# Kernel optimization log

Measured on AMD Instinct MI355X. Metric: run time of the kernel, lower is better.

Reference implementation:

```python
import jax, jax.numpy as jnp
import numpy as np
import math

FS = 9          # gaussian filter_size
STD = 1.0
LOW = 0.1       # min(threshold1, threshold2)
HIGH = 0.3      # max(threshold1, threshold2)
PAD_G = FS // 2


def _gauss_window(M, std):
    # scipy.signal.windows.gaussian: exp(-0.5*(n/std)^2), n centered, unnormalized
    n = np.arange(M, dtype=np.float64) - (M - 1) / 2.0
    return np.exp(-0.5 * (n / std) ** 2).astype(np.float32)


def _conv(x, w, pad):
    # torch F.conv2d == cross-correlation, NCHW / OIHW
    return jax.lax.conv_general_dilated(
        x, w, window_strides=(1, 1), padding=pad,
        dimension_numbers=("NCHW", "OIHW", "NCHW"))


def setup_inputs() -> dict:
    key = jax.random.key(0)
    img = jax.random.uniform(key, (8, 3, 512, 512), dtype=jnp.float32)
    g = _gauss_window(FS, STD)
    gauss_h = jnp.asarray(g[None, None, None, :])          # [1,1,1,9]
    gauss_v = jnp.asarray(g[None, None, :, None])          # [1,1,9,1]
    sobel_h = jnp.array([[[[1., 0., -1.], [2., 0., -2.], [1., 0., -1.]]]], dtype=jnp.float32)
    sobel_v = jnp.array([[[[1., 2., 1.], [0., 0., 0.], [-1., -2., -1.]]]], dtype=jnp.float32)
    d = np.zeros((8, 1, 3, 3), dtype=np.float32)
    d[:, 0, 1, 1] = 1.0
    # neighbor positions (row, col) for the -1 tap, per directional channel
    neigh = [(1, 2), (2, 2), (2, 1), (2, 0), (1, 0), (0, 0), (0, 1), (0, 2)]
    for k, (r, c) in enumerate(neigh):
        d[k, 0, r, c] = -1.0
    directional = jnp.asarray(d)                            # [8,1,3,3]
    connect = jnp.array([[[[1., 1., 1.], [1., 0., 1.], [1., 1., 1.]]]], dtype=jnp.float32)
    return {"img": img, "gauss_h": gauss_h, "gauss_v": gauss_v,
            "sobel_h": sobel_h, "sobel_v": sobel_v,
            "directional": directional, "connect": connect}


def reference(img, gauss_h, gauss_v, sobel_h, sobel_v, directional, connect):
    B, C, H, W = img.shape
    x = img.reshape(B * C, 1, H, W)  # per-channel 1-in/1-out convs, batched
    blur = _conv(_conv(x, gauss_h, [(0, 0), (PAD_G, PAD_G)]),
                 gauss_v, [(PAD_G, PAD_G), (0, 0)])
    gx = _conv(blur, sobel_h, [(1, 1), (1, 1)]).reshape(B, C, H, W)
    gy = _conv(blur, sobel_v, [(1, 1), (1, 1)]).reshape(B, C, H, W)

    # sum of per-channel magnitudes, [B,1,H,W]
    grad_mag = jnp.sqrt(gx * gx + gy * gy).sum(axis=1, keepdims=True)
    ori = jnp.arctan2(gy.sum(axis=1, keepdims=True),
                      gx.sum(axis=1, keepdims=True)) * (180.0 / math.pi) + 180.0
    ori = jnp.round(ori / 45.0) * 45.0

    all_filtered = _conv(grad_mag, directional, [(1, 1), (1, 1)])  # [B,8,H,W]

    pixel_count = B * H * W
    pr = jnp.arange(pixel_count, dtype=jnp.int32)
    flat = all_filtered.reshape(-1)
    # faithful replication of the original's flat linear-index gather
    k_pos = ((ori / 45.0) % 8.0).reshape(-1).astype(jnp.int32)
    k_neg = ((ori / 45.0 + 4.0) % 8.0).reshape(-1).astype(jnp.int32)
    pos = flat[k_pos * pixel_count + pr].reshape(B, 1, H, W)
    neg = flat[k_neg * pixel_count + pr].reshape(B, 1, H, W)

    is_max = jnp.minimum(pos, neg) > 0.0
    thin = jnp.where(is_max, grad_mag, 0.0)

    t = jnp.where(thin < LOW, 0.0, thin)
    higher = thin > HIGH
    t = jnp.where(higher, 1.0, t)
    connect_map = _conv(higher.astype(jnp.float32), connect, [(1, 1), (1, 1)])
    middle = (thin >= LOW) & (thin <= HIGH)
    t = jnp.where(middle, 0.0, t)
    connect_map = jnp.where(middle, connect_map, 0.0)
    t = jnp.where(connect_map > 0.0, 1.0, t)
    # zero borders
    t = t.at[..., 0, :].set(0.0)
    t = t.at[..., -1, :].set(0.0)
    t = t.at[..., :, 0].set(0.0)
    t = t.at[..., :, -1].set(0.0)
    return (t > 0.0).astype(jnp.float32)
```

## Files before the change

### kernel.cpp

```cpp
#include <hip/hip_runtime.h>
#include <math.h>

#define HH 512
#define WW 512
#define NB 8
#define NC 3
#define HW (HH*WW)

#define RSTRIP 16
#define CSTRIP 62
#define NROWS (HH/RSTRIP)
#define NCOLS ((WW + CSTRIP - 1)/CSTRIP)

__global__ __launch_bounds__(64) void canny_gm_kernel(
    const float* __restrict__ img, const float* __restrict__ gwin,
    double* __restrict__ GM, unsigned char* __restrict__ KP)
{
    const int lane = threadIdx.x;
    const int cs   = blockIdx.x % NCOLS;
    const int rs   = blockIdx.x / NCOLS;
    const int b    = blockIdx.y;

    const int R0 = rs * RSTRIP;
    const int c0 = cs * CSTRIP - 1;
    const int cl = c0 + lane;

    double g[9];
#pragma unroll
    for (int k = 0; k < 9; ++k) g[k] = (double)gwin[k];

    int cidx[9]; bool cmask[9];
#pragma unroll
    for (int k = 0; k < 9; ++k) {
        int cc = cl - 4 + k;
        cmask[k] = ((unsigned)cc < (unsigned)WW);
        int cc2 = cc < 0 ? 0 : cc;
        cidx[k] = cc2 > (WW - 1) ? (WW - 1) : cc2;
    }
    const bool lane_out = (lane >= 1) && (lane <= CSTRIP) && (cl < WW);
    const bool cml = ((unsigned)(cl - 1) < (unsigned)WW);
    const bool cmr = ((unsigned)(cl + 1) < (unsigned)WW);

    const float* ip0 = img + ((size_t)b * NC + 0) * HW;
    const float* ip1 = img + ((size_t)b * NC + 1) * HW;
    const float* ip2 = img + ((size_t)b * NC + 2) * HW;

    double hb[3][9];
    double vb[3][3];
#pragma unroll
    for (int c = 0; c < 3; ++c) {
#pragma unroll
        for (int k = 0; k < 9; ++k) hb[c][k] = 0.0;
#pragma unroll
        for (int k = 0; k < 3; ++k) vb[c][k] = 0.0;
    }

    const double t225 = 0.41421356237309503;
    const double t675 = 2.414213562373095;
    const int rEnd = R0 + RSTRIP + 4;

#pragma unroll 1
    for (int chunk = 0; chunk < 3; ++chunk) {
        const int rbase = R0 - 5 + 9 * chunk;
#pragma unroll
        for (int ph = 0; ph < 9; ++ph) {
            const int r = rbase + ph;
            if (r > rEnd) continue;

            if ((unsigned)r < (unsigned)HH) {
                const size_t ro = (size_t)r * WW;
                float v0[9], v1[9], v2[9];
#pragma unroll
                for (int k = 0; k < 9; ++k) {
                    v0[k] = ip0[ro + cidx[k]];
                    v1[k] = ip1[ro + cidx[k]];
                    v2[k] = ip2[ro + cidx[k]];
                }
                double a0 = 0.0, a1 = 0.0, a2 = 0.0;
#pragma unroll
                for (int k = 0; k < 9; ++k) {
                    a0 = fma(g[k], (double)(cmask[k] ? v0[k] : 0.0f), a0);
                    a1 = fma(g[k], (double)(cmask[k] ? v1[k] : 0.0f), a1);
                    a2 = fma(g[k], (double)(cmask[k] ? v2[k] : 0.0f), a2);
                }
                hb[0][ph] = a0; hb[1][ph] = a1; hb[2][ph] = a2;
            } else {
                hb[0][ph] = 0.0; hb[1][ph] = 0.0; hb[2][ph] = 0.0;
            }

            if (r - 4 >= R0 - 1) {
#pragma unroll
                for (int c = 0; c < 3; ++c) {
                    double acc = 0.0;
#pragma unroll
                    for (int k = 0; k < 9; ++k)
                        acc = fma(g[k], hb[c][(ph + 1 + k) % 9], acc);
                    vb[c][(ph + 2) % 3] = acc;
                }
            }

            const int ri = r - 5;
            if (ri >= R0) {
                const bool up = (ri >= 1), dn = (ri <= HH - 2);
                double mag = 0.0, sgx = 0.0, sgy = 0.0;
#pragma unroll
                for (int c = 0; c < 3; ++c) {
                    double top = up ? vb[c][ph % 3]       : 0.0;
                    double mid =      vb[c][(ph + 1) % 3];
                    double bot = dn ? vb[c][(ph + 2) % 3] : 0.0;
                    double tl_ = __shfl_up(top, 1), tr_ = __shfl_down(top, 1);
                    double ml_ = __shfl_up(mid, 1), mr_ = __shfl_down(mid, 1);
                    double bl_ = __shfl_up(bot, 1), br_ = __shfl_down(bot, 1);
                    double tl = cml ? tl_ : 0.0, tr = cmr ? tr_ : 0.0;
                    double ml = cml ? ml_ : 0.0, mr = cmr ? mr_ : 0.0;
                    double bl = cml ? bl_ : 0.0, br = cmr ? br_ : 0.0;
                    double tc = top, bc = bot;
                    double gx = (tl - tr) + 2.0*(ml - mr) + (bl - br);
                    double gy = (tl + 2.0*tc + tr) - (bl + 2.0*bc + br);
                    mag += sqrt(gx*gx + gy*gy);
                    sgx += gx; sgy += gy;
                }
                if (lane_out) {
                    size_t o = (size_t)b * HW + (size_t)ri * WW + cl;
                    GM[o] = mag;
                    double ax = fabs(sgx), ay = fabs(sgy);
                    int kp;
                    if (ay <= ax * t225)      kp = (sgx >= 0.0) ? 4 : 0;
                    else if (ay >= ax * t675) kp = (sgy > 0.0) ? 6 : 2;
                    else if (sgx > 0.0)       kp = (sgy > 0.0) ? 5 : 3;
                    else                      kp = (sgy > 0.0) ? 7 : 1;
                    KP[o] = (unsigned char)kp;
                }
            }
        }
    }
}

__global__ __launch_bounds__(256) void canny_thin_kernel(
    const double* __restrict__ GM, const unsigned char* __restrict__ KP,
    unsigned char* __restrict__ CODE)
{
    int idx = blockIdx.x * blockDim.x + threadIdx.x;
    if (idx >= NB * HW) return;
    int j = idx & (WW - 1);
    int i = (idx >> 9) & (HH - 1);
    int b = idx >> 18;

    int dr = (int)((0x00012221u >> (b * 4)) & 15u) - 1;
    int dc = (int)((0x21000122u >> (b * 4)) & 15u) - 1;

    int kp = KP[idx];
    int kn = (kp + 4) & 7;
    int ni = i + dr, nj = j + dc;
    bool nin = ((unsigned)ni < (unsigned)HH) && ((unsigned)nj < (unsigned)WW);
    size_t p0 = (size_t)i * WW + j;
    size_t pn = (size_t)ni * WW + nj;

    double gmp  = GM[(size_t)kp * HW + p0];
    double gmn  = GM[(size_t)kn * HW + p0];
    double gmpn = nin ? GM[(size_t)kp * HW + pn] : 0.0;
    double gmnn = nin ? GM[(size_t)kn * HW + pn] : 0.0;

    double pos = gmp - gmpn;
    double neg = gmn - gmnn;
    double thin = (fmin(pos, neg) > 0.0) ? GM[idx] : 0.0;

    unsigned char code = 0;
    if (thin > 0.3) code |= 1;
    if (thin >= 0.1 && thin <= 0.3) code |= 2;
    CODE[idx] = code;
}

__global__ __launch_bounds__(256) void canny_out_kernel(
    const unsigned char* __restrict__ CODE, float* __restrict__ out)
{
    int idx = blockIdx.x * blockDim.x + threadIdx.x;
    if (idx >= NB * HW) return;
    int j = idx & (WW - 1);
    int i = (idx >> 9) & (HH - 1);
    int b = idx >> 18;

    float r = 0.0f;
    if (i > 0 && i < HH - 1 && j > 0 && j < WW - 1) {
        unsigned char c = CODE[idx];
        if (c & 1) {
            r = 1.0f;
        } else if (c & 2) {
            const unsigned char* base = CODE + (size_t)b * HW;
            int any = 0;
            any |= base[(size_t)(i-1)*WW + (j-1)] & 1;
            any |= base[(size_t)(i-1)*WW + (j  )] & 1;
            any |= base[(size_t)(i-1)*WW + (j+1)] & 1;
            any |= base[(size_t)(i  )*WW + (j-1)] & 1;
            any |= base[(size_t)(i  )*WW + (j+1)] & 1;
            any |= base[(size_t)(i+1)*WW + (j-1)] & 1;
            any |= base[(size_t)(i+1)*WW + (j  )] & 1;
            any |= base[(size_t)(i+1)*WW + (j+1)] & 1;
            if (any) r = 1.0f;
        }
    }
    out[idx] = r;
}

extern "C" void kernel_launch(void* const* d_in, const int* in_sizes, int n_in,
                              void* d_out, int out_size, void* d_ws, size_t ws_size,
                              hipStream_t stream) {
    const float* img  = (const float*)d_in[0];
    const float* gwin = (const float*)d_in[1];

    double* GM = (double*)d_ws;
    unsigned char* KP = (unsigned char*)d_ws + (size_t)NB * HW * sizeof(double);
    unsigned char* CODE = KP + (size_t)NB * HW;
    float* out = (float*)d_out;

    dim3 g1(NCOLS * NROWS, NB);
    canny_gm_kernel<<<g1, 64, 0, stream>>>(img, gwin, GM, KP);

    int nblk = (NB * HW) / 256;
    canny_thin_kernel<<<nblk, 256, 0, stream>>>(GM, KP, CODE);
    canny_out_kernel<<<nblk, 256, 0, stream>>>(CODE, out);
}
```

Before: 77.26 us.

## Specialize gradient kernel for interior strips and pack four waves per block

Templates the gradient-magnitude strip on whether the column and row strips are interior, so interior strips skip clamping and masking and load rows with unaligned float4 vector loads. The row loop is unrolled into three fixed phases, which removes the runtime row-range checks. The Sobel stencil is factored into separable sums, so each channel needs four shuffles instead of six. Blocks now hold four wavefronts covering four row strips, giving fewer, larger blocks at the cost of more code and register pressure from the template variants.

Measured after the change: 96.22 us. 1.25x slower.

```diff
diff --git a/kernel.cpp b/kernel.cpp
--- a/kernel.cpp
+++ b/kernel.cpp
@@ -12,38 +12,32 @@
 #define NROWS (HH/RSTRIP)
 #define NCOLS ((WW + CSTRIP - 1)/CSTRIP)
 
-__global__ __launch_bounds__(64) void canny_gm_kernel(
-    const float* __restrict__ img, const float* __restrict__ gwin,
+typedef float float4u __attribute__((ext_vector_type(4), aligned(4)));
+
+template<bool CS, bool RS>
+__device__ __forceinline__ void gm_strip(
+    const float* __restrict__ ip0, const float* __restrict__ ip1,
+    const float* __restrict__ ip2, const double* g,
+    int lane, int R0, int cl, int b,
     double* __restrict__ GM, unsigned char* __restrict__ KP)
 {
-    const int lane = threadIdx.x;
-    const int cs   = blockIdx.x % NCOLS;
-    const int rs   = blockIdx.x / NCOLS;
-    const int b    = blockIdx.y;
-
-    const int R0 = rs * RSTRIP;
-    const int c0 = cs * CSTRIP - 1;
-    const int cl = c0 + lane;
-
-    double g[9];
-#pragma unroll
-    for (int k = 0; k < 9; ++k) g[k] = (double)gwin[k];
-
     int cidx[9]; bool cmask[9];
-#pragma unroll
-    for (int k = 0; k < 9; ++k) {
-        int cc = cl - 4 + k;
-        cmask[k] = ((unsigned)cc < (unsigned)WW);
-        int cc2 = cc < 0 ? 0 : cc;
-        cidx[k] = cc2 > (WW - 1) ? (WW - 1) : cc2;
-    }
-    const bool lane_out = (lane >= 1) && (lane <= CSTRIP) && (cl < WW);
-    const bool cml = ((unsigned)(cl - 1) < (unsigned)WW);
-    const bool cmr = ((unsigned)(cl + 1) < (unsigned)WW);
-
-    const float* ip0 = img + ((size_t)b * NC + 0) * HW;
-    const float* ip1 = img + ((size_t)b * NC + 1) * HW;
-    const float* ip2 = img + ((size_t)b * NC + 2) * HW;
+    bool cml, cmr, lane_out;
+    if (CS) {
+        cml = true; cmr = true;
+        lane_out = (lane >= 1) && (lane <= CSTRIP);
+    } else {
+#pragma unroll
+        for (int k = 0; k < 9; ++k) {
+            int cc = cl - 4 + k;
+            cmask[k] = ((unsigned)cc < (unsigned)WW);
+            int cc2 = cc < 0 ? 0 : cc;
+            cidx[k] = cc2 > (WW - 1) ? (WW - 1) : cc2;
+        }
+        cml = ((unsigned)(cl - 1) < (unsigned)WW);
+        cmr = ((unsigned)(cl + 1) < (unsigned)WW);
+        lane_out = (lane >= 1) && (lane <= CSTRIP) && (cl < WW);
+    }
 
     double hb[3][9];
     double vb[3][3];
@@ -57,18 +51,31 @@
 
     const double t225 = 0.41421356237309503;
     const double t675 = 2.414213562373095;
-    const int rEnd = R0 + RSTRIP + 4;
-
-#pragma unroll 1
-    for (int chunk = 0; chunk < 3; ++chunk) {
-        const int rbase = R0 - 5 + 9 * chunk;
-#pragma unroll
-        for (int ph = 0; ph < 9; ++ph) {
-            const int r = rbase + ph;
-            if (r > rEnd) continue;
-
-            if ((unsigned)r < (unsigned)HH) {
-                const size_t ro = (size_t)r * WW;
+
+    auto PHASE = [&](int r, int ph, bool doV, bool doS) {
+        bool rin = RS ? true : ((unsigned)r < (unsigned)HH);
+        if (rin) {
+            const size_t ro = (size_t)r * WW;
+            if (CS) {
+                const float* rp0 = ip0 + ro + (cl - 4);
+                const float* rp1 = ip1 + ro + (cl - 4);
+                const float* rp2 = ip2 + ro + (cl - 4);
+                float4u A0 = *(const float4u*)rp0, B0 = *(const float4u*)(rp0 + 4);
+                float4u A1 = *(const float4u*)rp1, B1 = *(const float4u*)(rp1 + 4);
+                float4u A2 = *(const float4u*)rp2, B2 = *(const float4u*)(rp2 + 4);
+                float e0 = rp0[8], e1 = rp1[8], e2 = rp2[8];
+                double a0 = 0.0, a1 = 0.0, a2 = 0.0;
+#pragma unroll
+                for (int k = 0; k < 9; ++k) {
+                    float v0 = k < 4 ? A0[k] : (k < 8 ? B0[k - 4] : e0);
+                    float v1 = k < 4 ? A1[k] : (k < 8 ? B1[k - 4] : e1);
+                    float v2 = k < 4 ? A2[k] : (k < 8 ? B2[k - 4] : e2);
+                    a0 = fma(g[k], (double)v0, a0);
+                    a1 = fma(g[k], (double)v1, a1);
+                    a2 = fma(g[k], (double)v2, a2);
+                }
+                hb[0][ph] = a0; hb[1][ph] = a1; hb[2][ph] = a2;
+            } else {
                 float v0[9], v1[9], v2[9];
 #pragma unroll
                 for (int k = 0; k < 9; ++k) {
@@ -84,55 +91,106 @@
                     a2 = fma(g[k], (double)(cmask[k] ? v2[k] : 0.0f), a2);
                 }
                 hb[0][ph] = a0; hb[1][ph] = a1; hb[2][ph] = a2;
-            } else {
-                hb[0][ph] = 0.0; hb[1][ph] = 0.0; hb[2][ph] = 0.0;
-            }
-
-            if (r - 4 >= R0 - 1) {
-#pragma unroll
-                for (int c = 0; c < 3; ++c) {
-                    double acc = 0.0;
-#pragma unroll
-                    for (int k = 0; k < 9; ++k)
-                        acc = fma(g[k], hb[c][(ph + 1 + k) % 9], acc);
-                    vb[c][(ph + 2) % 3] = acc;
-                }
-            }
-
+            }
+        } else {
+            hb[0][ph] = 0.0; hb[1][ph] = 0.0; hb[2][ph] = 0.0;
+        }
+
+        if (doV) {
+#pragma unroll
+            for (int c = 0; c < 3; ++c) {
+                double acc = 0.0;
+#pragma unroll
+                for (int k = 0; k < 9; ++k)
+                    acc = fma(g[k], hb[c][(ph + 1 + k) % 9], acc);
+                vb[c][(ph + 2) % 3] = acc;
+            }
+        }
+
+        if (doS) {
             const int ri = r - 5;
-            if (ri >= R0) {
-                const bool up = (ri >= 1), dn = (ri <= HH - 2);
-                double mag = 0.0, sgx = 0.0, sgy = 0.0;
-#pragma unroll
-                for (int c = 0; c < 3; ++c) {
-                    double top = up ? vb[c][ph % 3]       : 0.0;
-                    double mid =      vb[c][(ph + 1) % 3];
-                    double bot = dn ? vb[c][(ph + 2) % 3] : 0.0;
-                    double tl_ = __shfl_up(top, 1), tr_ = __shfl_down(top, 1);
-                    double ml_ = __shfl_up(mid, 1), mr_ = __shfl_down(mid, 1);
-                    double bl_ = __shfl_up(bot, 1), br_ = __shfl_down(bot, 1);
-                    double tl = cml ? tl_ : 0.0, tr = cmr ? tr_ : 0.0;
-                    double ml = cml ? ml_ : 0.0, mr = cmr ? mr_ : 0.0;
-                    double bl = cml ? bl_ : 0.0, br = cmr ? br_ : 0.0;
-                    double tc = top, bc = bot;
-                    double gx = (tl - tr) + 2.0*(ml - mr) + (bl - br);
-                    double gy = (tl + 2.0*tc + tr) - (bl + 2.0*bc + br);
-                    mag += sqrt(gx*gx + gy*gy);
-                    sgx += gx; sgy += gy;
-                }
-                if (lane_out) {
-                    size_t o = (size_t)b * HW + (size_t)ri * WW + cl;
-                    GM[o] = mag;
-                    double ax = fabs(sgx), ay = fabs(sgy);
-                    int kp;
-                    if (ay <= ax * t225)      kp = (sgx >= 0.0) ? 4 : 0;
-                    else if (ay >= ax * t675) kp = (sgy > 0.0) ? 6 : 2;
-                    else if (sgx > 0.0)       kp = (sgy > 0.0) ? 5 : 3;
-                    else                      kp = (sgy > 0.0) ? 7 : 1;
-                    KP[o] = (unsigned char)kp;
-                }
-            }
-        }
+            const bool up = RS ? true : (ri >= 1);
+            const bool dn = RS ? true : (ri <= HH - 2);
+            double mag = 0.0, sgx = 0.0, sgy = 0.0;
+#pragma unroll
+            for (int c = 0; c < 3; ++c) {
+                double top = up ? vb[c][ph % 3]       : 0.0;
+                double mid =      vb[c][(ph + 1) % 3];
+                double bot = dn ? vb[c][(ph + 2) % 3] : 0.0;
+                double s = top + 2.0 * mid + bot;
+                double d = top - bot;
+                double sL = __shfl_up(s, 1), sR = __shfl_down(s, 1);
+                double dL = __shfl_up(d, 1), dR = __shfl_down(d, 1);
+                if (!CS) {
+                    sL = cml ? sL : 0.0;  sR = cmr ? sR : 0.0;
+                    dL = cml ? dL : 0.0;  dR = cmr ? dR : 0.0;
+                }
+                double gx = sL - sR;
+                double gy = dL + 2.0 * d + dR;
+                mag += sqrt(gx * gx + gy * gy);
+                sgx += gx; sgy += gy;
+            }
+            if (lane_out) {
+                size_t o = (size_t)b * HW + (size_t)ri * WW + cl;
+                GM[o] = mag;
+                double ax = fabs(sgx), ay = fabs(sgy);
+                int kp;
+                if (ay <= ax * t225)      kp = (sgx >= 0.0) ? 4 : 0;
+                else if (ay >= ax * t675) kp = (sgy > 0.0) ? 6 : 2;
+                else if (sgx > 0.0)       kp = (sgy > 0.0) ? 5 : 3;
+                else                      kp = (sgy > 0.0) ? 7 : 1;
+                KP[o] = (unsigned char)kp;
+            }
+        }
+    };
+
+    {
+        const int rb = R0 - 5;
+#pragma unroll
+        for (int ph = 0; ph < 9; ++ph) PHASE(rb + ph, ph, ph == 8, false);
+    }
+    {
+        const int rb = R0 + 4;
+#pragma unroll
+        for (int ph = 0; ph < 9; ++ph) PHASE(rb + ph, ph, true, ph >= 1);
+    }
+    {
+        const int rb = R0 + 13;
+#pragma unroll
+        for (int ph = 0; ph < 8; ++ph) PHASE(rb + ph, ph, true, true);
+    }
+}
+
+__global__ __launch_bounds__(256) void canny_gm_kernel(
+    const float* __restrict__ img, const float* __restrict__ gwin,
+    double* __restrict__ GM, unsigned char* __restrict__ KP)
+{
+    const int lane = threadIdx.x & 63;
+    const int wv   = threadIdx.x >> 6;
+    const int cs   = blockIdx.x % NCOLS;
+    const int rs   = (blockIdx.x / NCOLS) * 4 + wv;
+    const int b    = blockIdx.y;
+
+    const int R0 = rs * RSTRIP;
+    const int cl = cs * CSTRIP - 1 + lane;
+
+    double g[9];
+#pragma unroll
+    for (int k = 0; k < 9; ++k) g[k] = (double)gwin[k];
+
+    const float* ip0 = img + ((size_t)b * NC + 0) * HW;
+    const float* ip1 = img + ((size_t)b * NC + 1) * HW;
+    const float* ip2 = img + ((size_t)b * NC + 2) * HW;
+
+    const bool csafe = (cs >= 1) && (cs <= NCOLS - 2);
+    const bool rsafe = (rs >= 1) && (rs <= NROWS - 2);
+
+    if (csafe) {
+        if (rsafe) gm_strip<true, true >(ip0, ip1, ip2, g, lane, R0, cl, b, GM, KP);
+        else       gm_strip<true, false>(ip0, ip1, ip2, g, lane, R0, cl, b, GM, KP);
+    } else {
+        if (rsafe) gm_strip<false, true >(ip0, ip1, ip2, g, lane, R0, cl, b, GM, KP);
+        else       gm_strip<false, false>(ip0, ip1, ip2, g, lane, R0, cl, b, GM, KP);
     }
 }
 
@@ -213,8 +271,8 @@
     unsigned char* CODE = KP + (size_t)NB * HW;
     float* out = (float*)d_out;
 
-    dim3 g1(NCOLS * NROWS, NB);
-    canny_gm_kernel<<<g1, 64, 0, stream>>>(img, gwin, GM, KP);
+    dim3 g1(NCOLS * (NROWS / 4), NB);
+    canny_gm_kernel<<<g1, 256, 0, stream>>>(img, gwin, GM, KP);
 
     int nblk = (NB * HW) / 256;
     canny_thin_kernel<<<nblk, 256, 0, stream>>>(GM, KP, CODE);
```

## Fuse thinning and hysteresis kernels via shared-memory tiles, halve row strip

Applied to the files above, without the earlier changes.

Merges the thinning and output kernels into one tiled kernel that computes threshold codes for a 34x34 halo tile in shared memory and then resolves 8-neighbour connectivity from LDS. This removes the CODE round trip through global memory and one launch, at the cost of recomputing the halo codes. The gradient kernel's row strip drops from 16 to 8 and becomes two fully unrolled 9-row phases. That doubles the block count but also raises the vertical halo overhead per output row. The Sobel step is factored into column sums and differences, cutting the shuffles per channel from six to four.

New measurement: 73.25 us. 5.2% less time.

```diff
diff --git a/kernel.cpp b/kernel.cpp
--- a/kernel.cpp
+++ b/kernel.cpp
@@ -7,7 +7,7 @@
 #define NC 3
 #define HW (HH*WW)
 
-#define RSTRIP 16
+#define RSTRIP 8
 #define CSTRIP 62
 #define NROWS (HH/RSTRIP)
 #define NCOLS ((WW + CSTRIP - 1)/CSTRIP)
@@ -22,8 +22,7 @@
     const int b    = blockIdx.y;
 
     const int R0 = rs * RSTRIP;
-    const int c0 = cs * CSTRIP - 1;
-    const int cl = c0 + lane;
+    const int cl = cs * CSTRIP - 1 + lane;
 
     double g[9];
 #pragma unroll
@@ -57,149 +56,154 @@
 
     const double t225 = 0.41421356237309503;
     const double t675 = 2.414213562373095;
-    const int rEnd = R0 + RSTRIP + 4;
-
-#pragma unroll 1
-    for (int chunk = 0; chunk < 3; ++chunk) {
-        const int rbase = R0 - 5 + 9 * chunk;
-#pragma unroll
-        for (int ph = 0; ph < 9; ++ph) {
-            const int r = rbase + ph;
-            if (r > rEnd) continue;
-
-            if ((unsigned)r < (unsigned)HH) {
-                const size_t ro = (size_t)r * WW;
-                float v0[9], v1[9], v2[9];
-#pragma unroll
-                for (int k = 0; k < 9; ++k) {
-                    v0[k] = ip0[ro + cidx[k]];
-                    v1[k] = ip1[ro + cidx[k]];
-                    v2[k] = ip2[ro + cidx[k]];
+
+    auto PHASE = [&](int r, int ph, bool doV, bool doS) {
+        if ((unsigned)r < (unsigned)HH) {
+            const size_t ro = (size_t)r * WW;
+            float v0[9], v1[9], v2[9];
+#pragma unroll
+            for (int k = 0; k < 9; ++k) {
+                v0[k] = ip0[ro + cidx[k]];
+                v1[k] = ip1[ro + cidx[k]];
+                v2[k] = ip2[ro + cidx[k]];
+            }
+            double a0 = 0.0, a1 = 0.0, a2 = 0.0;
+#pragma unroll
+            for (int k = 0; k < 9; ++k) {
+                a0 = fma(g[k], (double)(cmask[k] ? v0[k] : 0.0f), a0);
+                a1 = fma(g[k], (double)(cmask[k] ? v1[k] : 0.0f), a1);
+                a2 = fma(g[k], (double)(cmask[k] ? v2[k] : 0.0f), a2);
+            }
+            hb[0][ph] = a0; hb[1][ph] = a1; hb[2][ph] = a2;
+        } else {
+            hb[0][ph] = 0.0; hb[1][ph] = 0.0; hb[2][ph] = 0.0;
+        }
+
+        if (doV) {
+#pragma unroll
+            for (int c = 0; c < 3; ++c) {
+                double acc = 0.0;
+#pragma unroll
+                for (int k = 0; k < 9; ++k)
+                    acc = fma(g[k], hb[c][(ph + 1 + k) % 9], acc);
+                vb[c][(ph + 2) % 3] = acc;
+            }
+        }
+
+        if (doS) {
+            const int ri = r - 5;
+            const bool up = (ri >= 1), dn = (ri <= HH - 2);
+            double mag = 0.0, sgx = 0.0, sgy = 0.0;
+#pragma unroll
+            for (int c = 0; c < 3; ++c) {
+                double top = up ? vb[c][ph % 3]       : 0.0;
+                double mid =      vb[c][(ph + 1) % 3];
+                double bot = dn ? vb[c][(ph + 2) % 3] : 0.0;
+                double s = top + 2.0 * mid + bot;
+                double d = top - bot;
+                double sL = __shfl_up(s, 1), sR = __shfl_down(s, 1);
+                double dL = __shfl_up(d, 1), dR = __shfl_down(d, 1);
+                sL = cml ? sL : 0.0;  sR = cmr ? sR : 0.0;
+                dL = cml ? dL : 0.0;  dR = cmr ? dR : 0.0;
+                double gx = sL - sR;
+                double gy = dL + 2.0 * d + dR;
+                mag += sqrt(gx * gx + gy * gy);
+                sgx += gx; sgy += gy;
+            }
+            if (lane_out) {
+                size_t o = (size_t)b * HW + (size_t)ri * WW + cl;
+                GM[o] = mag;
+                double ax = fabs(sgx), ay = fabs(sgy);
+                int kp;
+                if (ay <= ax * t225)      kp = (sgx >= 0.0) ? 4 : 0;
+                else if (ay >= ax * t675) kp = (sgy > 0.0) ? 6 : 2;
+                else if (sgx > 0.0)       kp = (sgy > 0.0) ? 5 : 3;
+                else                      kp = (sgy > 0.0) ? 7 : 1;
+                KP[o] = (unsigned char)kp;
+            }
+        }
+    };
+
+    {
+        const int rb = R0 - 5;
+#pragma unroll
+        for (int ph = 0; ph < 9; ++ph) PHASE(rb + ph, ph, ph == 8, false);
+    }
+    {
+        const int rb = R0 + 4;
+#pragma unroll
+        for (int ph = 0; ph < 9; ++ph) PHASE(rb + ph, ph, true, ph >= 1);
+    }
+}
+
+__global__ __launch_bounds__(256) void canny_thin_out_kernel(
+    const double* __restrict__ GM, const unsigned char* __restrict__ KP,
+    float* __restrict__ out)
+{
+    __shared__ unsigned char scode[34 * 35];
+
+    const int tilesX = WW / 32;
+    const int tx0 = (blockIdx.x % tilesX) * 32;
+    const int ty0 = (blockIdx.x / tilesX) * 32;
+    const int b = blockIdx.y;
+    const int t = threadIdx.x;
+
+    const int dr = (int)((0x00012221u >> (b * 4)) & 15u) - 1;
+    const int dc = (int)((0x21000122u >> (b * 4)) & 15u) - 1;
+
+    {
+        int r = t / 34, cc = t % 34, idx = t;
+#pragma unroll
+        for (int it = 0; it < 5; ++it) {
+            if (idx < 34 * 34) {
+                int gi = ty0 - 1 + r, gj = tx0 - 1 + cc;
+                unsigned char code = 0;
+                if ((unsigned)gi < (unsigned)HH && (unsigned)gj < (unsigned)WW) {
+                    size_t p0 = (size_t)gi * WW + gj;
+                    int kp = KP[(size_t)b * HW + p0];
+                    int kn = (kp + 4) & 7;
+                    int ni = gi + dr, nj = gj + dc;
+                    bool nin = ((unsigned)ni < (unsigned)HH) && ((unsigned)nj < (unsigned)WW);
+                    size_t pn = (size_t)ni * WW + nj;
+                    double gmp  = GM[(size_t)kp * HW + p0];
+                    double gmn  = GM[(size_t)kn * HW + p0];
+                    double gmpn = nin ? GM[(size_t)kp * HW + pn] : 0.0;
+                    double gmnn = nin ? GM[(size_t)kn * HW + pn] : 0.0;
+                    double pos = gmp - gmpn;
+                    double neg = gmn - gmnn;
+                    double thin = (fmin(pos, neg) > 0.0) ? GM[(size_t)b * HW + p0] : 0.0;
+                    if (thin > 0.3) code |= 1;
+                    if (thin >= 0.1 && thin <= 0.3) code |= 2;
                 }
-                double a0 = 0.0, a1 = 0.0, a2 = 0.0;
-#pragma unroll
-                for (int k = 0; k < 9; ++k) {
-                    a0 = fma(g[k], (double)(cmask[k] ? v0[k] : 0.0f), a0);
-                    a1 = fma(g[k], (double)(cmask[k] ? v1[k] : 0.0f), a1);
-                    a2 = fma(g[k], (double)(cmask[k] ? v2[k] : 0.0f), a2);
-                }
-                hb[0][ph] = a0; hb[1][ph] = a1; hb[2][ph] = a2;
-            } else {
-                hb[0][ph] = 0.0; hb[1][ph] = 0.0; hb[2][ph] = 0.0;
-            }
-
-            if (r - 4 >= R0 - 1) {
-#pragma unroll
-                for (int c = 0; c < 3; ++c) {
-                    double acc = 0.0;
-#pragma unroll
-                    for (int k = 0; k < 9; ++k)
-                        acc = fma(g[k], hb[c][(ph + 1 + k) % 9], acc);
-                    vb[c][(ph + 2) % 3] = acc;
-                }
-            }
-
-            const int ri = r - 5;
-            if (ri >= R0) {
-                const bool up = (ri >= 1), dn = (ri <= HH - 2);
-                double mag = 0.0, sgx = 0.0, sgy = 0.0;
-#pragma unroll
-                for (int c = 0; c < 3; ++c) {
-                    double top = up ? vb[c][ph % 3]       : 0.0;
-                    double mid =      vb[c][(ph + 1) % 3];
-                    double bot = dn ? vb[c][(ph + 2) % 3] : 0.0;
-                    double tl_ = __shfl_up(top, 1), tr_ = __shfl_down(top, 1);
-                    double ml_ = __shfl_up(mid, 1), mr_ = __shfl_down(mid, 1);
-                    double bl_ = __shfl_up(bot, 1), br_ = __shfl_down(bot, 1);
-                    double tl = cml ? tl_ : 0.0, tr = cmr ? tr_ : 0.0;
-                    double ml = cml ? ml_ : 0.0, mr = cmr ? mr_ : 0.0;
-                    double bl = cml ? bl_ : 0.0, br = cmr ? br_ : 0.0;
-                    double tc = top, bc = bot;
-                    double gx = (tl - tr) + 2.0*(ml - mr) + (bl - br);
-                    double gy = (tl + 2.0*tc + tr) - (bl + 2.0*bc + br);
-                    mag += sqrt(gx*gx + gy*gy);
-                    sgx += gx; sgy += gy;
-                }
-                if (lane_out) {
-                    size_t o = (size_t)b * HW + (size_t)ri * WW + cl;
-                    GM[o] = mag;
-                    double ax = fabs(sgx), ay = fabs(sgy);
-                    int kp;
-                    if (ay <= ax * t225)      kp = (sgx >= 0.0) ? 4 : 0;
-                    else if (ay >= ax * t675) kp = (sgy > 0.0) ? 6 : 2;
-                    else if (sgx > 0.0)       kp = (sgy > 0.0) ? 5 : 3;
-                    else                      kp = (sgy > 0.0) ? 7 : 1;
-                    KP[o] = (unsigned char)kp;
-                }
-            }
-        }
-    }
-}
-
-__global__ __launch_bounds__(256) void canny_thin_kernel(
-    const double* __restrict__ GM, const unsigned char* __restrict__ KP,
-    unsigned char* __restrict__ CODE)
-{
-    int idx = blockIdx.x * blockDim.x + threadIdx.x;
-    if (idx >= NB * HW) return;
-    int j = idx & (WW - 1);
-    int i = (idx >> 9) & (HH - 1);
-    int b = idx >> 18;
-
-    int dr = (int)((0x00012221u >> (b * 4)) & 15u) - 1;
-    int dc = (int)((0x21000122u >> (b * 4)) & 15u) - 1;
-
-    int kp = KP[idx];
-    int kn = (kp + 4) & 7;
-    int ni = i + dr, nj = j + dc;
-    bool nin = ((unsigned)ni < (unsigned)HH) && ((unsigned)nj < (unsigned)WW);
-    size_t p0 = (size_t)i * WW + j;
-    size_t pn = (size_t)ni * WW + nj;
-
-    double gmp  = GM[(size_t)kp * HW + p0];
-    double gmn  = GM[(size_t)kn * HW + p0];
-    double gmpn = nin ? GM[(size_t)kp * HW + pn] : 0.0;
-    double gmnn = nin ? GM[(size_t)kn * HW + pn] : 0.0;
-
-    double pos = gmp - gmpn;
-    double neg = gmn - gmnn;
-    double thin = (fmin(pos, neg) > 0.0) ? GM[idx] : 0.0;
-
-    unsigned char code = 0;
-    if (thin > 0.3) code |= 1;
-    if (thin >= 0.1 && thin <= 0.3) code |= 2;
-    CODE[idx] = code;
-}
-
-__global__ __launch_bounds__(256) void canny_out_kernel(
-    const unsigned char* __restrict__ CODE, float* __restrict__ out)
-{
-    int idx = blockIdx.x * blockDim.x + threadIdx.x;
-    if (idx >= NB * HW) return;
-    int j = idx & (WW - 1);
-    int i = (idx >> 9) & (HH - 1);
-    int b = idx >> 18;
-
-    float r = 0.0f;
-    if (i > 0 && i < HH - 1 && j > 0 && j < WW - 1) {
-        unsigned char c = CODE[idx];
-        if (c & 1) {
-            r = 1.0f;
-        } else if (c & 2) {
-            const unsigned char* base = CODE + (size_t)b * HW;
-            int any = 0;
-            any |= base[(size_t)(i-1)*WW + (j-1)] & 1;
-            any |= base[(size_t)(i-1)*WW + (j  )] & 1;
-            any |= base[(size_t)(i-1)*WW + (j+1)] & 1;
-            any |= base[(size_t)(i  )*WW + (j-1)] & 1;
-            any |= base[(size_t)(i  )*WW + (j+1)] & 1;
-            any |= base[(size_t)(i+1)*WW + (j-1)] & 1;
-            any |= base[(size_t)(i+1)*WW + (j  )] & 1;
-            any |= base[(size_t)(i+1)*WW + (j+1)] & 1;
-            if (any) r = 1.0f;
-        }
-    }
-    out[idx] = r;
+                scode[r * 35 + cc] = code;
+            }
+            idx += 256; r += 7; cc += 18;
+            if (cc >= 34) { cc -= 34; ++r; }
+        }
+    }
+    __syncthreads();
+
+#pragma unroll
+    for (int p = 0; p < 4; ++p) {
+        int pix = t + p * 256;
+        int i = pix >> 5, j = pix & 31;
+        int gi = ty0 + i, gj = tx0 + j;
+        float res = 0.0f;
+        if (gi > 0 && gi < HH - 1 && gj > 0 && gj < WW - 1) {
+            const unsigned char* sc = scode + (i + 1) * 35 + (j + 1);
+            unsigned char c = *sc;
+            if (c & 1) {
+                res = 1.0f;
+            } else if (c & 2) {
+                int any = 0;
+                any |= sc[-36] & 1; any |= sc[-35] & 1; any |= sc[-34] & 1;
+                any |= sc[-1]  & 1; any |= sc[ 1]  & 1;
+                any |= sc[ 34] & 1; any |= sc[ 35] & 1; any |= sc[ 36] & 1;
+                if (any) res = 1.0f;
+            }
+        }
+        out[(size_t)b * HW + (size_t)gi * WW + gj] = res;
+    }
 }
 
 extern "C" void kernel_launch(void* const* d_in, const int* in_sizes, int n_in,
@@ -210,13 +214,11 @@
 
     double* GM = (double*)d_ws;
     unsigned char* KP = (unsigned char*)d_ws + (size_t)NB * HW * sizeof(double);
-    unsigned char* CODE = KP + (size_t)NB * HW;
     float* out = (float*)d_out;
 
     dim3 g1(NCOLS * NROWS, NB);
     canny_gm_kernel<<<g1, 64, 0, stream>>>(img, gwin, GM, KP);
 
-    int nblk = (NB * HW) / 256;
-    canny_thin_kernel<<<nblk, 256, 0, stream>>>(GM, KP, CODE);
-    canny_out_kernel<<<nblk, 256, 0, stream>>>(CODE, out);
+    dim3 g2((WW / 32) * (HH / 32), NB);
+    canny_thin_out_kernel<<<g2, 256, 0, stream>>>(GM, KP, out);
 }
```
